# Performance work log

Measured on AMD Instinct MI355X. Metric: run time of the kernel, lower is better.

## Reference

```python
import jax, jax.numpy as jnp
import numpy as np

MIN_DISTANCE = 31  # glimpse size (h, w)


def setup_inputs() -> dict:
    key = jax.random.key(0)
    k1, k2, k3 = jax.random.split(key, 3)
    B, N, C, H, W = 8, 600, 32, 256, 256
    images = jax.random.normal(k1, (B, C, H, W), dtype=jnp.float32)
    # anchor boxes (xmin, ymin, xmax, ymax) in pixel coords, kept in-bounds
    xy1 = jax.random.uniform(k2, (B, N, 2), dtype=jnp.float32) * (H - 64) + 16.0
    wh = jax.random.uniform(k3, (B, N, 2), dtype=jnp.float32) * 32.0 + 8.0
    anc_bases = jnp.concatenate([xy1, xy1 + wh], axis=-1)  # [B, N, 4]
    return {"images": images, "anc_bases": anc_bases}


def _grid_sample_bilinear_zeros(images, grid):
    """torch.nn.functional.grid_sample(mode='bilinear', padding_mode='zeros',
    align_corners=False), vectorized over an arbitrary flat sample dim.
    images: [B, C, H, W]; grid: [B, P, 2] normalized coords (x, y) in [-1, 1].
    Returns [B, C, P].
    """
    B, C, H, W = images.shape
    # unnormalize (align_corners=False)
    px = (grid[..., 0] + 1.0) * (W * 0.5) - 0.5  # [B, P]
    py = (grid[..., 1] + 1.0) * (H * 0.5) - 0.5
    x0 = jnp.floor(px)
    y0 = jnp.floor(py)
    fx = px - x0
    fy = py - y0
    x0i = x0.astype(jnp.int32)
    y0i = y0.astype(jnp.int32)
    x1i = x0i + 1
    y1i = y0i + 1

    imgf = images.reshape(B, C, H * W)

    def corner(yi, xi, wgt):
        valid = (yi >= 0) & (yi < H) & (xi >= 0) & (xi < W)
        yc = jnp.clip(yi, 0, H - 1)
        xc = jnp.clip(xi, 0, W - 1)
        idx = (yc * W + xc)[:, None, :]  # [B, 1, P]
        vals = jnp.take_along_axis(imgf, idx, axis=2)  # [B, C, P]
        w_eff = jnp.where(valid, wgt, 0.0)[:, None, :]
        return vals * w_eff

    out = (
        corner(y0i, x0i, (1.0 - fx) * (1.0 - fy))
        + corner(y0i, x1i, fx * (1.0 - fy))
        + corner(y1i, x0i, (1.0 - fx) * fy)
        + corner(y1i, x1i, fx * fy)
    )
    return out  # [B, C, P]


def _extract_glimpses(images, anc_centers, size):
    B, C, H, W = images.shape
    N = anc_centers.shape[1]
    h, w = size
    xs = jnp.arange(w, dtype=images.dtype) - (w - 1) / 2.0
    ys = jnp.arange(h, dtype=images.dtype) - (h - 1) / 2.0
    vy, vx = jnp.meshgrid(ys, xs, indexing="ij")  # [h, w]
    grid = jnp.stack([vx, vy], axis=-1)  # [h, w, 2] (x, y)
    # offsets_grid: [B, N, h, w, 2]
    og = anc_centers[:, :, None, None, :] + grid[None, None, ...]
    norm = jnp.asarray([W / 2.0, H / 2.0], dtype=images.dtype)
    g = (og - norm) / norm  # normalized for grid_sample
    g_flat = g.reshape(B, N * h * w, 2)
    out = _grid_sample_bilinear_zeros(images, g_flat)  # [B, C, N*h*w]
    rois = out.reshape(B, C, N, h, w).transpose(0, 2, 1, 3, 4)  # [B, N, C, h, w]
    return rois


def reference(images, anc_bases):
    # eval path of CornerProposal.forward (targets=None)
    # note original: (a[..., :2] + a[..., :2]) // 2 == floor(a[..., :2])
    anc_centers = (anc_bases[:, :, :2] + anc_bases[:, :, :2]) // 2.0
    rois = _extract_glimpses(
        images, anc_centers, size=(MIN_DISTANCE, MIN_DISTANCE)
    )
    return rois, anc_bases[:, :, :2]
```

## Files before the change

kernel.cpp:

```cpp
#include <hip/hip_runtime.h>

#define BB 8
#define NN 600
#define CC 32
#define HH 256
#define WW 256
#define GG 31
#define PP 32
#define PATCH (PP * PP)


typedef __attribute__((address_space(3))) void lds_void_t;
typedef const __attribute__((address_space(1))) void gmem_void_t;

__global__ __launch_bounds__(256, 8) void rois_kernel(const float* __restrict__ images,
                                                      const float* __restrict__ anc,
                                                      float* __restrict__ out,
                                                      float* __restrict__ out_anc) {
    __shared__ float patch[2][PATCH];

    const int bid = blockIdx.x;
    const int bn  = (bid & 7) * ((BB * NN) / 8) + (bid >> 3);
    const int b   = bn / NN;

    const int t    = threadIdx.x;
    const int wave = t >> 6;
    const int tr   = t >> 5;
    const int lcol = t & 31;

    const float ax = anc[bn * 4 + 0];
    const float ay = anc[bn * 4 + 1];
    const int x0 = (int)floorf(ax) - 16;
    const int y0 = (int)floorf(ay) - 16;

    if (t == 0) {
        out_anc[bn * 2 + 0] = ax;
        out_anc[bn * 2 + 1] = ay;
    }

    const size_t plane = (size_t)HH * WW;
    const float* gbase = images + (size_t)(b * CC) * plane
                       + (size_t)(y0 + tr) * WW + (x0 + lcol);
    float* outbase = out + (size_t)bn * CC * (GG * GG);

    {
        float* sb = &patch[0][64 * wave];
        #pragma unroll
        for (int k = 0; k < 4; ++k)
            __builtin_amdgcn_global_load_lds((gmem_void_t*)(gbase + (size_t)(8 * k) * WW),
                                             (lds_void_t*)(sb + 256 * k),
                                             4, 0, 0);
    }
    __syncthreads();

    #pragma unroll 1
    for (int c = 0; c < CC; ++c) {
        if (c + 1 < CC) {
            const float* gp = gbase + (size_t)(c + 1) * plane;
            float* sb2 = &patch[(c + 1) & 1][64 * wave];
            #pragma unroll
            for (int k = 0; k < 4; ++k)
                __builtin_amdgcn_global_load_lds((gmem_void_t*)(gp + (size_t)(8 * k) * WW),
                                                 (lds_void_t*)(sb2 + 256 * k),
                                                 4, 0, 0);
        }

        const float* sb = patch[c & 1];
        float* o = outbase + (size_t)c * (GG * GG);
        if (lcol < GG) {
            #pragma unroll
            for (int k = 0; k < 4; ++k) {
                const int r = 8 * k + tr;
                if (r < GG) {
                    const float* sp = sb + r * PP + lcol;
                    const float v = 0.25f * (sp[0] + sp[1] + sp[PP] + sp[PP + 1]);
                    __builtin_nontemporal_store(v, &o[r * GG + lcol]);
                }
            }
        }

        __syncthreads();
    }
}

extern "C" void kernel_launch(void* const* d_in, const int* in_sizes, int n_in,
                              void* d_out, int out_size, void* d_ws, size_t ws_size,
                              hipStream_t stream) {
    const float* images = (const float*)d_in[0];
    const float* anc    = (const float*)d_in[1];
    float* out = (float*)d_out;
    float* out_anchors = out + (size_t)BB * NN * CC * GG * GG;

    rois_kernel<<<BB * NN, 256, 0, stream>>>(images, anc, out, out_anchors);
}
```

Before: 691.2 us.

## Replace LDS double-buffered patch staging with per-wave direct loads and shuffles

Drops the LDS double buffer and the per-channel __syncthreads. Each wave now handles its own set of channels and reads the two neighbouring rows straight from global memory. The horizontal neighbour comes from a wave shuffle, and the launch-bounds occupancy hint is lowered from 8 to 4. This removes the block-wide barriers and the LDS traffic, but each image row is read twice from global/L2 and the stores are no longer nontemporal.

```diff
diff --git a/kernel.cpp b/kernel.cpp
--- a/kernel.cpp
+++ b/kernel.cpp
@@ -6,27 +6,21 @@
 #define HH 256
 #define WW 256
 #define GG 31
-#define PP 32
-#define PATCH (PP * PP)
 
 
-typedef __attribute__((address_space(3))) void lds_void_t;
-typedef const __attribute__((address_space(1))) void gmem_void_t;
-
-__global__ __launch_bounds__(256, 8) void rois_kernel(const float* __restrict__ images,
+__global__ __launch_bounds__(256, 4) void rois_kernel(const float* __restrict__ images,
                                                       const float* __restrict__ anc,
                                                       float* __restrict__ out,
                                                       float* __restrict__ out_anc) {
-    __shared__ float patch[2][PATCH];
-
     const int bid = blockIdx.x;
     const int bn  = (bid & 7) * ((BB * NN) / 8) + (bid >> 3);
     const int b   = bn / NN;
 
     const int t    = threadIdx.x;
     const int wave = t >> 6;
-    const int tr   = t >> 5;
-    const int lcol = t & 31;
+    const int lane = t & 63;
+    const int lrow = lane >> 5;
+    const int lcol = lane & 31;
 
     const float ax = anc[bn * 4 + 0];
     const float ay = anc[bn * 4 + 1];
@@ -39,47 +33,28 @@
     }
 
     const size_t plane = (size_t)HH * WW;
-    const float* gbase = images + (size_t)(b * CC) * plane
-                       + (size_t)(y0 + tr) * WW + (x0 + lcol);
+    const float* ibase = images + (size_t)(b * CC) * plane
+                       + (size_t)y0 * WW + (x0 + lcol);
     float* outbase = out + (size_t)bn * CC * (GG * GG);
 
-    {
-        float* sb = &patch[0][64 * wave];
+    #pragma unroll 1
+    for (int ci = 0; ci < 8; ++ci) {
+        const int c = wave + 4 * ci;
+        const float* ip = ibase + (size_t)c * plane;
+        float* o = outbase + (size_t)c * (GG * GG);
+
         #pragma unroll
-        for (int k = 0; k < 4; ++k)
-            __builtin_amdgcn_global_load_lds((gmem_void_t*)(gbase + (size_t)(8 * k) * WW),
-                                             (lds_void_t*)(sb + 256 * k),
-                                             4, 0, 0);
-    }
-    __syncthreads();
-
-    #pragma unroll 1
-    for (int c = 0; c < CC; ++c) {
-        if (c + 1 < CC) {
-            const float* gp = gbase + (size_t)(c + 1) * plane;
-            float* sb2 = &patch[(c + 1) & 1][64 * wave];
-            #pragma unroll
-            for (int k = 0; k < 4; ++k)
-                __builtin_amdgcn_global_load_lds((gmem_void_t*)(gp + (size_t)(8 * k) * WW),
-                                                 (lds_void_t*)(sb2 + 256 * k),
-                                                 4, 0, 0);
-        }
-
-        const float* sb = patch[c & 1];
-        float* o = outbase + (size_t)c * (GG * GG);
-        if (lcol < GG) {
-            #pragma unroll
-            for (int k = 0; k < 4; ++k) {
-                const int r = 8 * k + tr;
-                if (r < GG) {
-                    const float* sp = sb + r * PP + lcol;
-                    const float v = 0.25f * (sp[0] + sp[1] + sp[PP] + sp[PP + 1]);
-                    __builtin_nontemporal_store(v, &o[r * GG + lcol]);
-                }
+        for (int k = 0; k < 16; ++k) {
+            const int r = 2 * k + lrow;
+            if (r < GG) {
+                const float a  = ip[(size_t)r * WW];
+                const float bv = ip[(size_t)(r + 1) * WW];
+                const float s  = a + bv;
+                const float sr = __shfl_down(s, 1, 32);
+                if (lcol < GG)
+                    o[r * GG + lcol] = 0.25f * (s + sr);
             }
         }
-
-        __syncthreads();
     }
 }
 
```

Result: slower. 806.3 us (+16.7%).
